# Kernel tuning notes

Measured on AMD Instinct MI355X. Metric: run time of the kernel, lower is better.

## Reference

```python
import jax, jax.numpy as jnp
import numpy as np

EPS = 1e-6
NUM_HEADS = 16


def setup_inputs() -> dict:
    key = jax.random.key(0)
    ks = jax.random.split(key, 11)
    B, S, E = 2, 2048, 1024
    sc = 1.0 / np.sqrt(E)
    return {
        "x": jax.random.normal(ks[0], (B, S, E), dtype=jnp.float32),
        "Wq": jax.random.normal(ks[1], (E, E), dtype=jnp.float32) * sc,
        "bq": jax.random.normal(ks[2], (E,), dtype=jnp.float32) * 0.01,
        "Wk": jax.random.normal(ks[3], (E, E), dtype=jnp.float32) * sc,
        "bk": jax.random.normal(ks[4], (E,), dtype=jnp.float32) * 0.01,
        "Wv": jax.random.normal(ks[5], (E, E), dtype=jnp.float32) * sc,
        "bv": jax.random.normal(ks[6], (E,), dtype=jnp.float32) * 0.01,
        "Wp": jax.random.normal(ks[7], (E, E), dtype=jnp.float32) * sc,
        "bp": jax.random.normal(ks[8], (E,), dtype=jnp.float32) * 0.01,
        "gain": jax.random.uniform(ks[9], (E,), dtype=jnp.float32),
        "beta": jax.random.normal(ks[10], (E,), dtype=jnp.float32),
    }


def _layer_norm(x, gain, beta):
    # torch: (x - mean) / (std + eps) * gain + bias, std with Bessel correction
    mean = jnp.mean(x, axis=-1, keepdims=True)
    std = jnp.std(x, axis=-1, keepdims=True, ddof=1)
    return (x - mean) / (std + EPS) * gain + beta


def reference(x, Wq, bq, Wk, bk, Wv, bv, Wp, bp, gain, beta):
    B, S, E = x.shape
    H = NUM_HEADS
    D = E // H
    # QKV projections, split heads: [B,S,E] -> [B,H,S,D]
    def heads(y):
        return y.reshape(B, S, H, D).transpose(0, 2, 1, 3)
    q = heads(x @ Wq + bq)
    k = heads(x @ Wk + bk)
    v = heads(x @ Wv + bv)
    # scores [B,H,S,S], mask=None path (no causal mask applied in forward)
    scores = jnp.einsum("bhid,bhjd->bhij", q, k) / jnp.sqrt(jnp.float32(D))
    attn = jax.nn.softmax(scores, axis=-1)  # dropout is identity at eval
    y = jnp.einsum("bhij,bhjd->bhid", attn, v)
    y = y.transpose(0, 2, 1, 3).reshape(B, S, E)
    return _layer_norm(y @ Wp + bp, gain, beta)
```

## Files before the change

### kernel.cpp

```cpp
#include <hip/hip_runtime.h>
#include <hip/hip_bf16.h>
#include <math.h>

constexpr int Bc = 2;
constexpr int Sc = 2048;
constexpr int Ec = 1024;
constexpr int Hc = 16;
constexpr int Dc = 64;

typedef __attribute__((ext_vector_type(8))) short short8;
typedef __attribute__((ext_vector_type(4))) short short4v;
typedef __attribute__((ext_vector_type(2))) int int2v;
typedef __attribute__((ext_vector_type(4))) float f32x4;

__device__ inline unsigned short f2bf(float x) {
    __hip_bfloat16 h = __float2bfloat16(x);
    return *reinterpret_cast<unsigned short*>(&h);
}

__device__ inline f32x4 mfma16(short8 a, short8 b, f32x4 c) {
    return __builtin_amdgcn_mfma_f32_16x16x32_bf16(a, b, c, 0, 0, 0);
}

__device__ inline f32x4 mfma16k16(short4v a, short4v b, f32x4 c) {
#if __has_builtin(__builtin_amdgcn_mfma_f32_16x16x16bf16_1k)
    return __builtin_amdgcn_mfma_f32_16x16x16bf16_1k(a, b, c, 0, 0, 0);
#else
    f32x4 d;
    asm("v_mfma_f32_16x16x16_bf16 %0, %1, %2, %3"
        : "=v"(d) : "v"(a), "v"(b), "v"(c));
    return d;
#endif
}

__device__ inline float exp2_fast(float x) {
    float r;
    asm("v_exp_f32 %0, %1" : "=v"(r) : "v"(x));
    return r;
}

__device__ inline int cvt_pk_bf16(float lo, float hi) {
    int r;
    asm("v_cvt_pk_bf16_f32 %0, %1, %2" : "=v"(r) : "v"(lo), "v"(hi));
    return r;
}

__device__ inline void gload_lds16(const unsigned short* gsrc, unsigned short* ldst) {
    __builtin_amdgcn_global_load_lds(
        (const __attribute__((address_space(1))) unsigned int*)(const void*)gsrc,
        (__attribute__((address_space(3))) unsigned int*)(void*)ldst,
        16, 0, 0);
}

__global__ __launch_bounds__(256) void prep_kernel(
    const float* __restrict__ X, unsigned short* __restrict__ Xb,
    const float* __restrict__ W0, const float* __restrict__ W1,
    const float* __restrict__ W2, const float* __restrict__ W3,
    unsigned short* __restrict__ T0, unsigned short* __restrict__ T1,
    unsigned short* __restrict__ T2, unsigned short* __restrict__ T3)
{
    __shared__ unsigned short Ls[64][72];
    const int bid = blockIdx.x, t = threadIdx.x;
    if (bid < 2048) {
        int i = bid * 256 + t;
        const float4* src = (const float4*)(X + (size_t)i * 8);
        float4 a = src[0], b = src[1];
        short8 o;
        o[0] = f2bf(a.x); o[1] = f2bf(a.y); o[2] = f2bf(a.z); o[3] = f2bf(a.w);
        o[4] = f2bf(b.x); o[5] = f2bf(b.y); o[6] = f2bf(b.z); o[7] = f2bf(b.w);
        *(short8*)(Xb + (size_t)i * 8) = o;
        return;
    }
    const int tt = bid - 2048;
    const float* W; unsigned short* T;
    switch (tt >> 8) {
        case 0: W = W0; T = T0; break;
        case 1: W = W1; T = T1; break;
        case 2: W = W2; T = T2; break;
        default: W = W3; T = T3; break;
    }
    const int rem = tt & 255;
    const int n0 = (rem & 15) * 64, k0 = (rem >> 4) * 64;
    {
        int k = t >> 2, nb = (t & 3) * 16;
        const float* src = W + (size_t)(k0 + k) * Ec + n0 + nb;
#pragma unroll
        for (int j = 0; j < 16; ++j) Ls[k][nb + j] = f2bf(src[j]);
    }
    __syncthreads();
    {
        int n = t >> 2, kb = (t & 3) * 16;
        short8 o0, o1;
#pragma unroll
        for (int j = 0; j < 8; ++j) { o0[j] = Ls[kb + j][n]; o1[j] = Ls[kb + 8 + j][n]; }
        unsigned short* dst = T + (size_t)(n0 + n) * Ec + k0 + kb;
        *(short8*)dst = o0;
        *(short8*)(dst + 8) = o1;
    }
}

constexpr int BM = 128, BK = 64;

template<int BNt>
__device__ __forceinline__ void gemm_core_t(
    const unsigned short* __restrict__ A, const unsigned short* __restrict__ Bt,
    const float* __restrict__ bias, float* __restrict__ Cf,
    unsigned short* __restrict__ Cb, int M, int N, int K, int mode, float oscale)
{
    constexpr int NW = BNt / 32;
    constexpr int WN = BNt / 2;
    constexpr int CH = (BM + BNt) / 8;
    constexpr int PW = CH / 4;
    __shared__ unsigned short lds[2][(BM + BNt) * BK];
    const int tid = threadIdx.x, lane = tid & 63, wid = tid >> 6;
    const int c16 = lane & 15, g = lane >> 4;
    const int wr = wid >> 1, wc = wid & 1;
    const int row0 = blockIdx.y * BM, col0 = blockIdx.x * BNt;

    const int rsub = lane >> 3;
    const int colE = ((lane & 7) ^ rsub) * 8;

    f32x4 acc[4][NW] = {};

    auto stage = [&](int buf, int k0) {
        unsigned short* Ab = &lds[buf][0];
        unsigned short* Bb = &lds[buf][BM * BK];
#pragma unroll
        for (int i = 0; i < PW; ++i) {
            int c = wid * PW + i;
            if (c < 16) {
                const unsigned short* src = A + (size_t)(row0 + c * 8 + rsub) * K + k0 + colE;
                gload_lds16(src, Ab + c * 512);
            } else {
                int c2 = c - 16;
                const unsigned short* src = Bt + (size_t)(col0 + c2 * 8 + rsub) * K + k0 + colE;
                gload_lds16(src, Bb + c2 * 512);
            }
        }
    };

    stage(0, 0);
    __syncthreads();
    int cur = 0;
    const int NT = K / BK;
    for (int t = 0; t < NT; ++t) {
        if (t + 1 < NT) stage(cur ^ 1, (t + 1) * BK);
        const unsigned short* Ab = &lds[cur][0];
        const unsigned short* Bb = &lds[cur][BM * BK];
#pragma unroll
        for (int kk = 0; kk < 2; ++kk) {
            const int cb = ((kk * 64 + g * 16) ^ ((c16 & 7) << 4)) >> 1;
            short8 af[4], bfr[NW];
#pragma unroll
            for (int m = 0; m < 4; ++m) {
                int row = wr * 64 + m * 16 + c16;
                af[m] = *(const short8*)(Ab + row * BK + cb);
            }
#pragma unroll
            for (int n = 0; n < NW; ++n) {
                int row = wc * WN + n * 16 + c16;
                bfr[n] = *(const short8*)(Bb + row * BK + cb);
            }
#pragma unroll
            for (int m = 0; m < 4; ++m)
#pragma unroll
                for (int n = 0; n < NW; ++n)
                    acc[m][n] = mfma16(af[m], bfr[n], acc[m][n]);
        }
        __syncthreads();
        cur ^= 1;
    }

#pragma unroll
    for (int m = 0; m < 4; ++m) {
#pragma unroll
        for (int n = 0; n < NW; ++n) {
            int gc = col0 + wc * WN + n * 16 + c16;
            float bi = bias[gc];
            if (mode == 2) {
                int h = gc >> 6, d = gc & (Dc - 1);
                int s0 = row0 + wr * 64 + m * 16 + g * 4;
                int b = s0 >> 11, s = s0 & (Sc - 1);
                short4v pk;
#pragma unroll
                for (int r = 0; r < 4; ++r)
                    pk[r] = (short)f2bf((acc[m][n][r] + bi) * oscale);
                *(short4v*)&Cb[(((size_t)b * Hc + h) * Dc + d) * Sc + s] = pk;
            } else {
#pragma unroll
                for (int r = 0; r < 4; ++r) {
                    int gr = row0 + wr * 64 + m * 16 + g * 4 + r;
                    float v = (acc[m][n][r] + bi) * oscale;
                    if (mode == 0) {
                        Cf[(size_t)gr * N + gc] = v;
                    } else {
                        int b = gr >> 11, s = gr & (Sc - 1);
                        int h = gc >> 6, d = gc & (Dc - 1);
                        Cb[(((size_t)b * Hc + h) * Sc + s) * Dc + d] = f2bf(v);
                    }
                }
            }
        }
    }
}

__global__ __launch_bounds__(256) void gemm_mfma_kernel(
    const unsigned short* __restrict__ A, const unsigned short* __restrict__ Bt,
    const float* __restrict__ bias, float* __restrict__ Cf, int M, int N, int K)
{
    gemm_core_t<64>(A, Bt, bias, Cf, nullptr, M, N, K, 0, 1.0f);
}

__global__ __launch_bounds__(256) void qkv_gemm_kernel(
    const unsigned short* __restrict__ A,
    const unsigned short* __restrict__ WqT, const unsigned short* __restrict__ WkT,
    const unsigned short* __restrict__ WvT,
    const float* __restrict__ bq, const float* __restrict__ bk,
    const float* __restrict__ bv,
    unsigned short* __restrict__ Qb, unsigned short* __restrict__ Kb,
    unsigned short* __restrict__ Vt, int M, int N, int K, float sl2e)
{
    if (blockIdx.z == 0)      gemm_core_t<128>(A, WqT, bq, nullptr, Qb, M, N, K, 1, sl2e);
    else if (blockIdx.z == 1) gemm_core_t<128>(A, WkT, bk, nullptr, Kb, M, N, K, 1, 1.0f);
    else                      gemm_core_t<128>(A, WvT, bv, nullptr, Vt, M, N, K, 2, 1.0f);
}

__global__ __launch_bounds__(256) void attn_mfma_kernel(
    const unsigned short* __restrict__ Q, const unsigned short* __restrict__ K,
    const unsigned short* __restrict__ Vt, unsigned short* __restrict__ Y)
{
    __shared__ __align__(16) unsigned short lds[2][2][64 * 64];

    const int tid  = threadIdx.x;
    const int lane = tid & 63, wid = tid >> 6;
    const int g = lane >> 4, c16 = lane & 15;
    const int bh = blockIdx.x;
    const int qw = blockIdx.y * 128 + wid * 32;
    const size_t base = (size_t)bh * Sc * Dc;

    short8 bq[2][2];
#pragma unroll
    for (int u = 0; u < 2; ++u) {
        const unsigned short* Qp = Q + base + (size_t)(qw + u * 16 + c16) * Dc;
        bq[u][0] = *(const short8*)(Qp + g * 8);
        bq[u][1] = *(const short8*)(Qp + 32 + g * 8);
    }

    const int rsub = lane >> 3;
    const int srcoffE = 8 * ((lane & 7) ^ rsub);
    const int row0g = (wid * 2 + 0) * 8 + rsub;
    const int row1g = (wid * 2 + 1) * 8 + rsub;

    const unsigned short* kg0 = K  + base + (size_t)row0g * Dc + srcoffE;
    const unsigned short* kg1 = K  + base + (size_t)row1g * Dc + srcoffE;
    const unsigned short* vg0 = Vt + base + (size_t)row0g * Sc + srcoffE;
    const unsigned short* vg1 = Vt + base + (size_t)row1g * Sc + srcoffE;

    f32x4 o[2][4] = {};
    float psacc[2] = {0.f, 0.f};

    auto stage = [&](unsigned short* kbuf, unsigned short* vbuf) {
        gload_lds16(kg0, kbuf + (wid * 2 + 0) * 512);
        gload_lds16(kg1, kbuf + (wid * 2 + 1) * 512);
        gload_lds16(vg0, vbuf + (wid * 2 + 0) * 512);
        gload_lds16(vg1, vbuf + (wid * 2 + 1) * 512);
        kg0 += 64 * Dc; kg1 += 64 * Dc;
        vg0 += 64;      vg1 += 64;
    };

    const int sw = (c16 & 7) << 4;

    auto compute = [&](const unsigned short* kbuf, const unsigned short* vbuf) {
        const char* kbc = (const char*)kbuf;
        const char* vbc = (const char*)vbuf;

        f32x4 c[2][4];
        __builtin_amdgcn_s_setprio(1);
#pragma unroll
        for (int ct = 0; ct < 4; ++ct) {
            const int kr = ct * 16 + c16;
            short8 alo = *(const short8*)(kbc + kr * 128 + ((16 * g) ^ sw));
            short8 ahi = *(const short8*)(kbc + kr * 128 + ((64 + 16 * g) ^ sw));
            f32x4 z0 = {}, z1 = {};
            z0 = mfma16(alo, bq[0][0], z0);
            c[0][ct] = mfma16(ahi, bq[0][1], z0);
            z1 = mfma16(alo, bq[1][0], z1);
            c[1][ct] = mfma16(ahi, bq[1][1], z1);
        }
        __builtin_amdgcn_s_setprio(0);

        short4v pbv[2][4];
#pragma unroll
        for (int u = 0; u < 2; ++u) {
            float ps = 0.f;
#pragma unroll
            for (int ct = 0; ct < 4; ++ct) {
                float p0 = exp2_fast(c[u][ct][0]);
                float p1 = exp2_fast(c[u][ct][1]);
                float p2 = exp2_fast(c[u][ct][2]);
                float p3 = exp2_fast(c[u][ct][3]);
                ps += (p0 + p1) + (p2 + p3);
                int2v w;
                w[0] = cvt_pk_bf16(p0, p1);
                w[1] = cvt_pk_bf16(p2, p3);
                pbv[u][ct] = __builtin_bit_cast(short4v, w);
            }
            psacc[u] += ps;
        }

        __builtin_amdgcn_s_setprio(1);
#pragma unroll
        for (int dt = 0; dt < 4; ++dt) {
            const int drow = dt * 16 + c16;
#pragma unroll
            for (int ct = 0; ct < 4; ++ct) {
                short4v va = *(const short4v*)(vbc + drow * 128 + ((ct * 32 + 8 * g) ^ sw));
                o[0][dt] = mfma16k16(va, pbv[0][ct], o[0][dt]);
                o[1][dt] = mfma16k16(va, pbv[1][ct], o[1][dt]);
            }
        }
        __builtin_amdgcn_s_setprio(0);
    };

    unsigned short* k0b = &lds[0][0][0]; unsigned short* v0b = &lds[0][1][0];
    unsigned short* k1b = &lds[1][0][0]; unsigned short* v1b = &lds[1][1][0];

    constexpr int NT = Sc / 64;
    stage(k0b, v0b);
    for (int kt = 0; kt < NT; kt += 2) {
        asm volatile("s_waitcnt vmcnt(0)" ::: "memory");
        __builtin_amdgcn_s_barrier();
        __builtin_amdgcn_sched_barrier(0);
        if (kt + 1 < NT) stage(k1b, v1b);
        compute(k0b, v0b);
        asm volatile("s_waitcnt vmcnt(0)" ::: "memory");
        __builtin_amdgcn_s_barrier();
        __builtin_amdgcn_sched_barrier(0);
        if (kt + 2 < NT) stage(k0b, v0b);
        compute(k1b, v1b);
    }

    const int b = bh >> 4, h = bh & (Hc - 1);
#pragma unroll
    for (int u = 0; u < 2; ++u) {
        float ps = psacc[u];
        ps += __shfl_xor(ps, 16);
        ps += __shfl_xor(ps, 32);
        const float inv = 1.f / ps;
        const int qg = qw + u * 16 + c16;
        unsigned short* yrow = Y + ((size_t)b * Sc + qg) * Ec + h * Dc;
#pragma unroll
        for (int dt = 0; dt < 4; ++dt)
#pragma unroll
            for (int r = 0; r < 4; ++r)
                yrow[dt * 16 + g * 4 + r] = f2bf(o[u][dt][r] * inv);
    }
}

__global__ __launch_bounds__(256) void ln_kernel(
    const float* __restrict__ Z, const float* __restrict__ gain,
    const float* __restrict__ beta, float* __restrict__ out)
{
    __shared__ float red0[4];
    __shared__ float red1[4];
    const int row = blockIdx.x;
    const int t = threadIdx.x;
    const float4* z4 = (const float4*)(Z + (size_t)row * Ec);
    float4 v = z4[t];

    float s = v.x + v.y + v.z + v.w;
#pragma unroll
    for (int off = 32; off > 0; off >>= 1) s += __shfl_down(s, off);
    if ((t & 63) == 0) red0[t >> 6] = s;
    __syncthreads();
    float mean = (red0[0] + red0[1] + red0[2] + red0[3]) * (1.0f / Ec);

    float dx = v.x - mean; float vs = dx * dx;
    dx = v.y - mean; vs += dx * dx;
    dx = v.z - mean; vs += dx * dx;
    dx = v.w - mean; vs += dx * dx;
#pragma unroll
    for (int off = 32; off > 0; off >>= 1) vs += __shfl_down(vs, off);
    if ((t & 63) == 0) red1[t >> 6] = vs;
    __syncthreads();
    float var = (red1[0] + red1[1] + red1[2] + red1[3]) * (1.0f / (Ec - 1));
    float inv = 1.0f / (sqrtf(var) + 1e-6f);

    float4 g = ((const float4*)gain)[t];
    float4 bb = ((const float4*)beta)[t];
    float4 o;
    o.x = (v.x - mean) * inv * g.x + bb.x;
    o.y = (v.y - mean) * inv * g.y + bb.y;
    o.z = (v.z - mean) * inv * g.z + bb.z;
    o.w = (v.w - mean) * inv * g.w + bb.w;
    ((float4*)(out + (size_t)row * Ec))[t] = o;
}

extern "C" void kernel_launch(void* const* d_in, const int* in_sizes, int n_in,
                              void* d_out, int out_size, void* d_ws, size_t ws_size,
                              hipStream_t stream)
{
    const float* x    = (const float*)d_in[0];
    const float* Wq   = (const float*)d_in[1];
    const float* bq   = (const float*)d_in[2];
    const float* Wk   = (const float*)d_in[3];
    const float* bk   = (const float*)d_in[4];
    const float* Wv   = (const float*)d_in[5];
    const float* bv   = (const float*)d_in[6];
    const float* Wp   = (const float*)d_in[7];
    const float* bp   = (const float*)d_in[8];
    const float* gain = (const float*)d_in[9];
    const float* beta = (const float*)d_in[10];

    const int M = Bc * Sc;
    const size_t MK  = (size_t)M * Ec;
    const size_t EE  = (size_t)Ec * Ec;

    unsigned short* xb  = (unsigned short*)d_ws;
    unsigned short* wqt = xb + MK;
    unsigned short* wkt = wqt + EE;
    unsigned short* wvt = wkt + EE;
    unsigned short* wpt = wvt + EE;
    unsigned short* qb  = wpt + EE;
    unsigned short* kb  = qb + MK;
    unsigned short* vt  = kb + MK;
    unsigned short* yb  = vt + MK;

    float* z = (float*)qb;

    const float sl2e = 0.125f * 1.44269504f;

    prep_kernel<<<3072, 256, 0, stream>>>(x, xb, Wq, Wk, Wv, Wp, wqt, wkt, wvt, wpt);

    dim3 qkv_grid(Ec / 128, M / BM, 3);
    qkv_gemm_kernel<<<qkv_grid, 256, 0, stream>>>(
        xb, wqt, wkt, wvt, bq, bk, bv, qb, kb, vt, M, Ec, Ec, sl2e);

    dim3 attn_grid(Bc * Hc, Sc / 128);
    attn_mfma_kernel<<<attn_grid, 256, 0, stream>>>(qb, kb, vt, yb);

    dim3 proj_grid(Ec / 64, M / BM);
    gemm_mfma_kernel<<<proj_grid, 256, 0, stream>>>(yb, wpt, bp, z, M, Ec, Ec);

    ln_kernel<<<M, 256, 0, stream>>>(z, gain, beta, (float*)d_out);
}
```

Measured before the change: 127.4 us.

## Use K=32 bf16 MFMA for PV by permuting V's sequence layout

The P·V product in the attention kernel switches from 16x16x16 bf16 MFMAs to 16x16x32 MFMAs, halving the number of MFMA issues and V LDS reads (now 16-byte loads). To make the packed P fragments line up with the wider K dimension, the V projection epilogue writes the transposed V with a permuted sequence index inside each group of 32, so the V layout in global memory is deliberately reordered to match the register layout of P. This couples the projection kernel's store pattern to the attention kernel's fragment layout.

```diff
diff --git a/kernel.cpp b/kernel.cpp
--- a/kernel.cpp
+++ b/kernel.cpp
@@ -10,7 +10,7 @@
 
 typedef __attribute__((ext_vector_type(8))) short short8;
 typedef __attribute__((ext_vector_type(4))) short short4v;
-typedef __attribute__((ext_vector_type(2))) int int2v;
+typedef __attribute__((ext_vector_type(4))) int int4v;
 typedef __attribute__((ext_vector_type(4))) float f32x4;
 
 __device__ inline unsigned short f2bf(float x) {
@@ -20,17 +20,6 @@
 
 __device__ inline f32x4 mfma16(short8 a, short8 b, f32x4 c) {
     return __builtin_amdgcn_mfma_f32_16x16x32_bf16(a, b, c, 0, 0, 0);
-}
-
-__device__ inline f32x4 mfma16k16(short4v a, short4v b, f32x4 c) {
-#if __has_builtin(__builtin_amdgcn_mfma_f32_16x16x16bf16_1k)
-    return __builtin_amdgcn_mfma_f32_16x16x16bf16_1k(a, b, c, 0, 0, 0);
-#else
-    f32x4 d;
-    asm("v_mfma_f32_16x16x16_bf16 %0, %1, %2, %3"
-        : "=v"(d) : "v"(a), "v"(b), "v"(c));
-    return d;
-#endif
 }
 
 __device__ inline float exp2_fast(float x) {
@@ -180,7 +169,9 @@
             if (mode == 2) {
                 int h = gc >> 6, d = gc & (Dc - 1);
                 int s0 = row0 + wr * 64 + m * 16 + g * 4;
-                int b = s0 >> 11, s = s0 & (Sc - 1);
+                int a = (s0 >> 2) & 7;
+                int sp = (s0 & ~31) + ((a & 3) << 3) + ((a >> 2) << 2);
+                int b = s0 >> 11, s = sp & (Sc - 1);
                 short4v pk;
 #pragma unroll
                 for (int r = 0; r < 4; ++r)
@@ -289,7 +280,7 @@
         }
         __builtin_amdgcn_s_setprio(0);
 
-        short4v pbv[2][4];
+        int4v p32[2][2];
 #pragma unroll
         for (int u = 0; u < 2; ++u) {
             float ps = 0.f;
@@ -300,10 +291,8 @@
                 float p2 = exp2_fast(c[u][ct][2]);
                 float p3 = exp2_fast(c[u][ct][3]);
                 ps += (p0 + p1) + (p2 + p3);
-                int2v w;
-                w[0] = cvt_pk_bf16(p0, p1);
-                w[1] = cvt_pk_bf16(p2, p3);
-                pbv[u][ct] = __builtin_bit_cast(short4v, w);
+                p32[u][ct >> 1][(ct & 1) * 2 + 0] = cvt_pk_bf16(p0, p1);
+                p32[u][ct >> 1][(ct & 1) * 2 + 1] = cvt_pk_bf16(p2, p3);
             }
             psacc[u] += ps;
         }
@@ -313,10 +302,10 @@
         for (int dt = 0; dt < 4; ++dt) {
             const int drow = dt * 16 + c16;
 #pragma unroll
-            for (int ct = 0; ct < 4; ++ct) {
-                short4v va = *(const short4v*)(vbc + drow * 128 + ((ct * 32 + 8 * g) ^ sw));
-                o[0][dt] = mfma16k16(va, pbv[0][ct], o[0][dt]);
-                o[1][dt] = mfma16k16(va, pbv[1][ct], o[1][dt]);
+            for (int w = 0; w < 2; ++w) {
+                short8 va = *(const short8*)(vbc + drow * 128 + ((w * 64 + 16 * g) ^ sw));
+                o[0][dt] = mfma16(va, __builtin_bit_cast(short8, p32[0][w]), o[0][dt]);
+                o[1][dt] = mfma16(va, __builtin_bit_cast(short8, p32[1][w]), o[1][dt]);
             }
         }
         __builtin_amdgcn_s_setprio(0);
```

Result: faster. 118.6 us (-6.9%).
